# Performance work log

Hardware: AMD Instinct MI355X
Metric: run time of the kernel (lower is better)

The kernel has to match this reference:

```python
import jax, jax.numpy as jnp
import numpy as np

E = 64            # embedding_size
N = 131072        # total nodes (64 states x 2048 objects)
B = 64            # number of states (for readout)
NUM_LAYERS = 2
SMOOTH = 12.0     # MAXIMUM_SMOOTHNESS
RELS = (("r1", 1, 400_000), ("r2", 2, 400_000), ("r3", 3, 150_000))  # (name, arity, n_atoms)


def mish(x):
    return x * jnp.tanh(jax.nn.softplus(x))


def mlp(x, Wi, bi, Wo, bo):
    # MLP: outer(mish(inner(x)))
    return mish(x @ Wi + bi) @ Wo + bo


def setup_inputs() -> dict:
    key = jax.random.key(0)
    ks = iter(jax.random.split(key, 64))

    def lin(i, o):
        s = 1.0 / np.sqrt(i)
        return jax.random.uniform(next(ks), (i, o), jnp.float32, -s, s)

    d = {"node_embeddings": jax.random.normal(next(ks), (N, E), jnp.float32)}
    for r, a, m in RELS:
        d[f"atoms_{r}"] = jax.random.randint(next(ks), (m * a,), 0, N, jnp.int32)
    d["token_sizes"] = jnp.full((B,), N // B, jnp.int32)
    for r, a, _ in RELS:
        sz = a * E
        d[f"Wi_{r}"] = lin(sz, sz); d[f"bi_{r}"] = jnp.zeros((sz,), jnp.float32)
        d[f"Wo_{r}"] = lin(sz, sz); d[f"bo_{r}"] = jnp.zeros((sz,), jnp.float32)
    d["uWi"] = lin(2 * E, 2 * E); d["ubi"] = jnp.zeros((2 * E,), jnp.float32)
    d["uWo"] = lin(2 * E, E);     d["ubo"] = jnp.zeros((E,), jnp.float32)
    for p in ("v", "d"):
        d[f"{p}Wi"] = lin(E, E); d[f"{p}bi"] = jnp.zeros((E,), jnp.float32)
        d[f"{p}Wo"] = lin(E, 1); d[f"{p}bo"] = jnp.zeros((1,), jnp.float32)
    return d


def _layer(h, atoms, rp, uWi, ubi, uWo, ubo):
    # per-relation gather -> residual MLP -> flatten back to per-term messages
    msg_list, idx_list = [], []
    for (r, a, _) in RELS:
        idx = atoms[r]                                  # [m*a] int node ids
        Wi, bi, Wo, bo = rp[r]
        x = h[idx].reshape(-1, a * E)                   # [m, a*E]
        y = x + mlp(x, Wi, bi, Wo, bo)                  # residual relation MLP
        msg_list.append(y.reshape(-1, E))               # [m*a, E]
        idx_list.append(idx)
    msgs = jnp.concatenate(msg_list, 0)                 # [T, E]
    idxs = jnp.concatenate(idx_list, 0)                 # [T]

    # smooth-max aggregation (torch: index_reduce amax under no_grad + stabilized exp-sum-log)
    cnt = jax.ops.segment_sum(jnp.ones((idxs.shape[0], 1), msgs.dtype), idxs, num_segments=N)
    seg_max = jax.ops.segment_max(msgs, idxs, num_segments=N)     # -inf for empty segments
    exps_max = jax.lax.stop_gradient(jnp.where(cnt > 0, seg_max, 0.0))  # include_self=False; empty nodes stay 0
    exps = jnp.exp(SMOOTH * (msgs - exps_max[idxs]))
    exps_sum = 1e-16 + jax.ops.segment_sum(exps, idxs, num_segments=N)
    max_msg = jnp.log(exps_sum) / SMOOTH + exps_max     # [N, E]

    return h + mlp(jnp.concatenate([max_msg, h], 1), uWi, ubi, uWo, ubo)


def _readout(h, token_sizes, Wi, bi, Wo, bo):
    # SumReadout: cumsum-diff segment sums over states, then MLP -> scalar per state
    ci = jnp.cumsum(token_sizes) - 1
    cs = jnp.cumsum(h, axis=0)[ci]                      # [B, E] cumulative sums at segment ends
    agg = jnp.concatenate([cs[:1], cs[1:] - cs[:-1]], 0)
    return mlp(agg, Wi, bi, Wo, bo).reshape(-1)


def _forward(node_embeddings, atoms, token_sizes, params):
    (rp, uWi, ubi, uWo, ubo, vWi, vbi, vWo, vbo, dWi, dbi, dWo, dbo) = params
    h = node_embeddings
    for _ in range(NUM_LAYERS):
        h = _layer(h, atoms, rp, uWi, ubi, uWo, ubo)
    values = _readout(h, token_sizes, vWi, vbi, vWo, vbo)
    deadends = _readout(h, token_sizes, dWi, dbi, dWo, dbo)
    return values, deadends


def reference(node_embeddings, atoms_r1, atoms_r2, atoms_r3, token_sizes,
              Wi_r1, bi_r1, Wo_r1, bo_r1,
              Wi_r2, bi_r2, Wo_r2, bo_r2,
              Wi_r3, bi_r3, Wo_r3, bo_r3,
              uWi, ubi, uWo, ubo,
              vWi, vbi, vWo, vbo,
              dWi, dbi, dWo, dbo):
    atoms = {"r1": atoms_r1, "r2": atoms_r2, "r3": atoms_r3}
    rp = {"r1": (Wi_r1, bi_r1, Wo_r1, bo_r1),
          "r2": (Wi_r2, bi_r2, Wo_r2, bo_r2),
          "r3": (Wi_r3, bi_r3, Wo_r3, bo_r3)}
    params = (rp, uWi, ubi, uWo, ubo, vWi, vbi, vWo, vbo, dWi, dbi, dWo, dbo)
    return _forward(node_embeddings, atoms, token_sizes, params)
```

## Files before the change

kernel.cpp:

```cpp
#include <hip/hip_runtime.h>
#include <math.h>

#define N_NODES 131072
#define NSTATES 64
#define NH ((size_t)N_NODES * 64)

typedef short bf16x8 __attribute__((ext_vector_type(8)));
typedef float f32x4 __attribute__((ext_vector_type(4)));

__device__ __forceinline__ ushort f2bf(float f) {
    unsigned u = __float_as_uint(f);
    return (ushort)((u + 0x7fffu + ((u >> 16) & 1u)) >> 16);
}
__device__ __forceinline__ float bf2f(ushort h) {
    return __uint_as_float(((unsigned)h) << 16);
}
__device__ __forceinline__ float mishf(float x) {
    if (x > 30.f) return x;
    float t = __builtin_amdgcn_exp2f(1.4426950408889634f * x);
    float r = t * t + 2.f * t;
    return x * r * __builtin_amdgcn_rcpf(r + 2.f);
}
__device__ __forceinline__ unsigned enc_f(float f) {
    unsigned u = __float_as_uint(f);
    return (u & 0x80000000u) ? ~u : (u | 0x80000000u);
}
__device__ __forceinline__ float dec_f(unsigned k) {
    unsigned u = (k & 0x80000000u) ? (k & 0x7fffffffu) : ~k;
    return __uint_as_float(u);
}

__device__ __forceinline__ bf16x8 load8f(const float* p) {
    const float4* q = (const float4*)p;
    float4 v0 = q[0], v1 = q[1];
    bf16x8 u;
    u[0] = (short)f2bf(v0.x); u[1] = (short)f2bf(v0.y);
    u[2] = (short)f2bf(v0.z); u[3] = (short)f2bf(v0.w);
    u[4] = (short)f2bf(v1.x); u[5] = (short)f2bf(v1.y);
    u[6] = (short)f2bf(v1.z); u[7] = (short)f2bf(v1.w);
    return u;
}

__global__ __launch_bounds__(256) void h2bf_kernel(
    const float* __restrict__ h, ushort* __restrict__ hb)
{
    size_t i = ((size_t)blockIdx.x * 256 + threadIdx.x) * 8;
    if (i >= NH) return;
    *(bf16x8*)(hb + i) = load8f(h + i);
}

struct WtJob  { const float* src; ushort* dst; int K; int Nc; int start; };
struct WtJobs { WtJob j[8]; int total; };

__global__ __launch_bounds__(256) void wt_conv_all_kernel(WtJobs jobs)
{
    int i = blockIdx.x * 256 + threadIdx.x;
    if (i >= jobs.total) return;
    int jj = 0;
    #pragma unroll
    for (int k = 1; k < 8; k++) if (i >= jobs.j[k].start) jj = k;
    WtJob jb = jobs.j[jj];
    int local = i - jb.start;
    int o = local / jb.K, k = local % jb.K;
    jb.dst[(size_t)o * jb.K + k] = f2bf(jb.src[(size_t)k * jb.Nc + o]);
}

__global__ __launch_bounds__(256) void count_kernel(
    const int* __restrict__ atoms, int T, unsigned* __restrict__ cnt)
{
    int i = blockIdx.x * 256 + threadIdx.x;
    if (i < T) atomicAdd(&cnt[atoms[i]], 1u);
}

__global__ __launch_bounds__(256) void scan1_kernel(
    const unsigned* __restrict__ cnt, unsigned* __restrict__ base,
    unsigned* __restrict__ totals)
{
    __shared__ unsigned sm[256];
    int t = threadIdx.x, blk = blockIdx.x;
    int i0 = blk * 512;
    unsigned a = cnt[i0 + 2 * t], bb = cnt[i0 + 2 * t + 1];
    unsigned p = a + bb;
    sm[t] = p;
    __syncthreads();
    for (int off = 1; off < 256; off <<= 1) {
        unsigned v = (t >= off) ? sm[t - off] : 0u;
        __syncthreads();
        sm[t] += v;
        __syncthreads();
    }
    unsigned incl = sm[t];
    base[i0 + 2 * t]     = incl - p;
    base[i0 + 2 * t + 1] = incl - p + a;
    if (t == 255) totals[blk] = sm[255];
}

__global__ __launch_bounds__(256) void scan2_kernel(
    unsigned* __restrict__ base, unsigned* __restrict__ pos,
    const unsigned* __restrict__ totals)
{
    __shared__ unsigned ps[4];
    int t = threadIdx.x, blk = blockIdx.x;
    int lane = t & 63, wv = t >> 6;
    unsigned v = (t < blk) ? totals[t] : 0u;
    #pragma unroll
    for (int o = 32; o >= 1; o >>= 1) v += (unsigned)__shfl_xor((int)v, o);
    if (lane == 0) ps[wv] = v;
    __syncthreads();
    unsigned off = ps[0] + ps[1] + ps[2] + ps[3];
    int i0 = blk * 512;
    unsigned b0 = base[i0 + 2 * t] + off;
    unsigned b1 = base[i0 + 2 * t + 1] + off;
    base[i0 + 2 * t]     = b0;  pos[i0 + 2 * t]     = b0;
    base[i0 + 2 * t + 1] = b1;  pos[i0 + 2 * t + 1] = b1;
}

template<int ARITY, int MODE>
__global__ __launch_bounds__(256, (ARITY == 3) ? 3 : 4)
void rel_kernel(const ushort* __restrict__ h, const int* __restrict__ atoms,
                const ushort* __restrict__ WiT, const float* __restrict__ bi,
                const ushort* __restrict__ WoT, const float* __restrict__ bo,
                unsigned* __restrict__ pos, ushort* __restrict__ y_sorted,
                unsigned* __restrict__ enc, float* __restrict__ exps, int m)
{
    constexpr int AE  = ARITY * 64;
    constexpr int BM  = 64;
    constexpr int NTW = AE / 64;
    constexpr int KS  = AE / 32;
    constexpr int S   = AE * 2;
    __shared__ __align__(16) ushort xs[BM * AE];
    __shared__ __align__(16) ushort ts[BM * AE];
    __shared__ unsigned slot_sm[BM * ARITY];
    const int tid = threadIdx.x, lane = tid & 63, wv = tid >> 6;
    const int a0 = blockIdx.x * BM;

    for (int task = tid; task < BM * (AE / 8); task += 256) {
        int r  = task / (AE / 8);
        int c8 = task % (AE / 8);
        int atom = a0 + r;
        bf16x8 u = {0, 0, 0, 0, 0, 0, 0, 0};
        if (atom < m) {
            int node = atoms[atom * ARITY + (c8 >> 3)];
            u = *(const bf16x8*)(h + (size_t)node * 64 + (size_t)(c8 & 7) * 8);
        }
        *(bf16x8*)((char*)xs + r * S + ((c8 * 16) ^ ((r & 7) << 4))) = u;
    }
    __syncthreads();

    const int cw0 = wv * NTW * 16;
    const int kg  = (lane >> 4) * 8;
    const int cl  = lane & 15;

    f32x4 acc[4][NTW];
    #pragma unroll
    for (int n = 0; n < NTW; n++) {
        float b = bi[cw0 + n * 16 + cl];
        #pragma unroll
        for (int a = 0; a < 4; a++) acc[a][n] = (f32x4){b, b, b, b};
    }
    #pragma unroll
    for (int ks = 0; ks < KS; ks++) {
        bf16x8 bf[NTW];
        #pragma unroll
        for (int n = 0; n < NTW; n++)
            bf[n] = *(const bf16x8*)(WiT + (size_t)(cw0 + n * 16 + cl) * AE + ks * 32 + kg);
        #pragma unroll
        for (int a = 0; a < 4; a++) {
            int row = a * 16 + cl;
            bf16x8 af = *(const bf16x8*)((char*)xs + row * S + (((ks * 32 + kg) * 2) ^ ((row & 7) << 4)));
            #pragma unroll
            for (int n = 0; n < NTW; n++)
                acc[a][n] = __builtin_amdgcn_mfma_f32_16x16x32_bf16(af, bf[n], acc[a][n], 0, 0, 0);
        }
    }
    #pragma unroll
    for (int a = 0; a < 4; a++)
        #pragma unroll
        for (int n = 0; n < NTW; n++)
            #pragma unroll
            for (int j = 0; j < 4; j++) {
                int row = a * 16 + (lane >> 4) * 4 + j;
                int col = cw0 + n * 16 + cl;
                *(ushort*)((char*)ts + row * S + ((col * 2) ^ ((row & 7) << 4))) = f2bf(mishf(acc[a][n][j]));
            }
    __syncthreads();

    #pragma unroll
    for (int n = 0; n < NTW; n++) {
        float b = bo[cw0 + n * 16 + cl];
        #pragma unroll
        for (int a = 0; a < 4; a++) acc[a][n] = (f32x4){b, b, b, b};
    }
    #pragma unroll
    for (int ks = 0; ks < KS; ks++) {
        bf16x8 bf[NTW];
        #pragma unroll
        for (int n = 0; n < NTW; n++)
            bf[n] = *(const bf16x8*)(WoT + (size_t)(cw0 + n * 16 + cl) * AE + ks * 32 + kg);
        #pragma unroll
        for (int a = 0; a < 4; a++) {
            int row = a * 16 + cl;
            bf16x8 af = *(const bf16x8*)((char*)ts + row * S + (((ks * 32 + kg) * 2) ^ ((row & 7) << 4)));
            #pragma unroll
            for (int n = 0; n < NTW; n++)
                acc[a][n] = __builtin_amdgcn_mfma_f32_16x16x32_bf16(af, bf[n], acc[a][n], 0, 0, 0);
        }
    }
    #pragma unroll
    for (int a = 0; a < 4; a++)
        #pragma unroll
        for (int n = 0; n < NTW; n++)
            #pragma unroll
            for (int j = 0; j < 4; j++) {
                int row = a * 16 + (lane >> 4) * 4 + j;
                int col = cw0 + n * 16 + cl;
                ushort* xp = (ushort*)((char*)xs + row * S + ((col * 2) ^ ((row & 7) << 4)));
                *xp = f2bf(bf2f(*xp) + acc[a][n][j]);
            }
    __syncthreads();

    const int nrows = BM * ARITY;
    if (MODE == 0) {
        if (tid < nrows) {
            int grow = a0 * ARITY + tid;
            unsigned s = 0u;
            if (grow < m * ARITY) s = atomicAdd(&pos[atoms[grow]], 1u);
            slot_sm[tid] = s;
        }
        __syncthreads();
        for (int rr = wv; rr < nrows; rr += 4) {
            int grow = a0 * ARITY + rr;
            if (grow >= m * ARITY) break;
            int r = rr / ARITY, c = (rr % ARITY) * 64 + lane;
            ushort yu = *(ushort*)((char*)xs + r * S + ((c * 2) ^ ((r & 7) << 4)));
            y_sorted[(size_t)slot_sm[rr] * 64 + lane] = yu;
        }
    } else {
        for (int rr = wv; rr < nrows; rr += 4) {
            int grow = a0 * ARITY + rr;
            if (grow >= m * ARITY) break;
            int node = atoms[grow];
            int r = rr / ARITY, c = (rr % ARITY) * 64 + lane;
            ushort yu = *(ushort*)((char*)xs + r * S + ((c * 2) ^ ((r & 7) << 4)));
            if (MODE == 1) {
                atomicMax(&enc[(size_t)node * 64 + lane], enc_f(bf2f(yu)));
            } else {
                size_t cell = (size_t)node * 64 + lane;
                float mx = dec_f(enc[cell]);
                atomicAdd(&exps[cell], __builtin_amdgcn_exp2f(17.312340490667562f * (bf2f(yu) - mx)));
            }
        }
    }
}

#define KSM 17.312340490667562f
__global__ __launch_bounds__(256) void aggregate_kernel(
    const ushort* __restrict__ y_sorted, const unsigned* __restrict__ base,
    const unsigned* __restrict__ cnt, unsigned* __restrict__ pos,
    ushort* __restrict__ mm)
{
    int node = blockIdx.x * 4 + (threadIdx.x >> 6);
    int lane = threadIdx.x & 63;
    unsigned b = base[node], c = cnt[node];
    if (lane == 0) pos[node] = b;
    const ushort* p = y_sorted + (size_t)b * 64 + lane;

    float m = -3.402823466e38f;
    float s = 0.f;
    unsigned j = 0;
    for (; j + 4 <= c; j += 4) {
        float a0 = bf2f(p[(size_t)(j + 0) * 64]);
        float a1 = bf2f(p[(size_t)(j + 1) * 64]);
        float a2 = bf2f(p[(size_t)(j + 2) * 64]);
        float a3 = bf2f(p[(size_t)(j + 3) * 64]);
        float q  = fmaxf(fmaxf(a0, a1), fmaxf(a2, a3));
        float mn = fmaxf(m, q);
        s = s * __builtin_amdgcn_exp2f(KSM * (m - mn))
          + __builtin_amdgcn_exp2f(KSM * (a0 - mn))
          + __builtin_amdgcn_exp2f(KSM * (a1 - mn))
          + __builtin_amdgcn_exp2f(KSM * (a2 - mn))
          + __builtin_amdgcn_exp2f(KSM * (a3 - mn));
        m = mn;
    }
    for (; j < c; j++) {
        float a  = bf2f(p[(size_t)j * 64]);
        float mn = fmaxf(m, a);
        s = s * __builtin_amdgcn_exp2f(KSM * (m - mn))
          + __builtin_amdgcn_exp2f(KSM * (a - mn));
        m = mn;
    }
    float me = c ? m : 0.f;
    float r = __builtin_amdgcn_logf(1e-16f + s) * 0.05776226504666211f + me;
    mm[(size_t)node * 64 + lane] = f2bf(r);
}

__global__ __launch_bounds__(256) void finalize_mm_kernel(
    const unsigned* __restrict__ enc, const float* __restrict__ exps,
    ushort* __restrict__ mm)
{
    size_t i = (size_t)blockIdx.x * 256 + threadIdx.x;
    if (i >= NH) return;
    unsigned key = enc[i];
    float mx = key ? dec_f(key) : 0.f;
    float r = __builtin_amdgcn_logf(1e-16f + exps[i]) * 0.05776226504666211f + mx;
    mm[i] = f2bf(r);
}

__global__ __launch_bounds__(256, 4)
void update_kernel(ushort* __restrict__ hio, const ushort* __restrict__ mm,
                   const ushort* __restrict__ uWiT, const float* __restrict__ ubi,
                   const ushort* __restrict__ uWoT, const float* __restrict__ ubo)
{
    constexpr int AE = 128, BM = 64, S = 256, NTW = 2, KS = 4;
    __shared__ __align__(16) ushort xs[BM * AE];
    __shared__ __align__(16) ushort ts[BM * AE];
    const int tid = threadIdx.x, lane = tid & 63, wv = tid >> 6;
    const int n0 = blockIdx.x * BM;

    for (int task = tid; task < BM * 16; task += 256) {
        int r = task >> 4, c8 = task & 15;
        int node = n0 + r;
        bf16x8 u;
        if (c8 < 8) u = *(const bf16x8*)(mm  + (size_t)node * 64 + c8 * 8);
        else        u = *(const bf16x8*)(hio + (size_t)node * 64 + (size_t)(c8 - 8) * 8);
        *(bf16x8*)((char*)xs + r * S + ((c8 * 16) ^ ((r & 7) << 4))) = u;
    }
    __syncthreads();

    const int cw0 = wv * NTW * 16;
    const int kg  = (lane >> 4) * 8;
    const int cl  = lane & 15;

    f32x4 acc[4][NTW];
    #pragma unroll
    for (int n = 0; n < NTW; n++) {
        float b = ubi[cw0 + n * 16 + cl];
        #pragma unroll
        for (int a = 0; a < 4; a++) acc[a][n] = (f32x4){b, b, b, b};
    }
    #pragma unroll
    for (int ks = 0; ks < KS; ks++) {
        bf16x8 bf[NTW];
        #pragma unroll
        for (int n = 0; n < NTW; n++)
            bf[n] = *(const bf16x8*)(uWiT + (size_t)(cw0 + n * 16 + cl) * AE + ks * 32 + kg);
        #pragma unroll
        for (int a = 0; a < 4; a++) {
            int row = a * 16 + cl;
            bf16x8 af = *(const bf16x8*)((char*)xs + row * S + (((ks * 32 + kg) * 2) ^ ((row & 7) << 4)));
            #pragma unroll
            for (int n = 0; n < NTW; n++)
                acc[a][n] = __builtin_amdgcn_mfma_f32_16x16x32_bf16(af, bf[n], acc[a][n], 0, 0, 0);
        }
    }
    #pragma unroll
    for (int a = 0; a < 4; a++)
        #pragma unroll
        for (int n = 0; n < NTW; n++)
            #pragma unroll
            for (int j = 0; j < 4; j++) {
                int row = a * 16 + (lane >> 4) * 4 + j;
                int col = cw0 + n * 16 + cl;
                *(ushort*)((char*)ts + row * S + ((col * 2) ^ ((row & 7) << 4))) = f2bf(mishf(acc[a][n][j]));
            }
    __syncthreads();

    f32x4 acc2[4];
    {
        float b = ubo[wv * 16 + cl];
        #pragma unroll
        for (int a = 0; a < 4; a++) acc2[a] = (f32x4){b, b, b, b};
    }
    #pragma unroll
    for (int ks = 0; ks < KS; ks++) {
        bf16x8 bf = *(const bf16x8*)(uWoT + (size_t)(wv * 16 + cl) * AE + ks * 32 + kg);
        #pragma unroll
        for (int a = 0; a < 4; a++) {
            int row = a * 16 + cl;
            bf16x8 af = *(const bf16x8*)((char*)ts + row * S + (((ks * 32 + kg) * 2) ^ ((row & 7) << 4)));
            acc2[a] = __builtin_amdgcn_mfma_f32_16x16x32_bf16(af, bf, acc2[a], 0, 0, 0);
        }
    }
    #pragma unroll
    for (int a = 0; a < 4; a++)
        #pragma unroll
        for (int j = 0; j < 4; j++) {
            int row = a * 16 + (lane >> 4) * 4 + j;
            int col = wv * 16 + cl;
            int hc = 64 + col;
            float hold = bf2f(*(ushort*)((char*)xs + row * S + ((hc * 2) ^ ((row & 7) << 4))));
            hio[(size_t)(n0 + row) * 64 + col] = f2bf(hold + acc2[a][j]);
        }
}

__global__ __launch_bounds__(64) void offsets_kernel(
    const int* __restrict__ toksz, int* __restrict__ off)
{
    int lane = threadIdx.x;
    int v = toksz[lane];
    int inc = v;
    #pragma unroll
    for (int o = 1; o < 64; o <<= 1) {
        int t = __shfl_up(inc, o);
        if (lane >= o) inc += t;
    }
    off[lane] = inc - v;
}

#define RCHUNK 32
__global__ __launch_bounds__(256) void readout_partial_kernel(
    const ushort* __restrict__ h, const int* __restrict__ toksz,
    const int* __restrict__ off, float* __restrict__ part)
{
    int s = blockIdx.x >> 5, c = blockIdx.x & (RCHUNK - 1);
    int cntr = toksz[s];
    int rpc = (cntr + RCHUNK - 1) / RCHUNK;
    int r0 = c * rpc;
    int r1 = min(r0 + rpc, cntr);
    int col = threadIdx.x & 63, rg = threadIdx.x >> 6;
    int base = off[s];
    float acc = 0.f;
    for (int r = r0 + rg; r < r1; r += 4)
        acc += bf2f(h[(size_t)(base + r) * 64 + col]);
    __shared__ float red[4][64];
    red[rg][col] = acc;
    __syncthreads();
    if (rg == 0)
        part[(size_t)blockIdx.x * 64 + col] = red[0][col] + red[1][col] + red[2][col] + red[3][col];
}

__global__ __launch_bounds__(256) void readout_reduce_kernel(
    const float* __restrict__ part, float* __restrict__ agg)
{
    int s = blockIdx.x;
    int col = threadIdx.x & 63, rg = threadIdx.x >> 6;
    float acc = 0.f;
    for (int k = rg; k < RCHUNK; k += 4)
        acc += part[(size_t)(s * RCHUNK + k) * 64 + col];
    __shared__ float red[4][64];
    red[rg][col] = acc;
    __syncthreads();
    if (rg == 0)
        agg[s * 64 + col] = red[0][col] + red[1][col] + red[2][col] + red[3][col];
}

__global__ __launch_bounds__(64) void readout_mlp_kernel(
    const float* __restrict__ agg,
    const float* __restrict__ vWi, const float* __restrict__ vbi,
    const float* __restrict__ vWo, const float* __restrict__ vbo,
    const float* __restrict__ dWi, const float* __restrict__ dbi,
    const float* __restrict__ dWo, const float* __restrict__ dbo,
    float* __restrict__ out)
{
    int s = blockIdx.x;
    int lane = threadIdx.x;
    float accv = vbi[lane], accd = dbi[lane];
    for (int k = 0; k < 64; k++) {
        float a = agg[s * 64 + k];
        accv = fmaf(a, vWi[k * 64 + lane], accv);
        accd = fmaf(a, dWi[k * 64 + lane], accd);
    }
    float pv = mishf(accv) * vWo[lane];
    float pd = mishf(accd) * dWo[lane];
    #pragma unroll
    for (int o = 1; o < 64; o <<= 1) {
        pv += __shfl_xor(pv, o);
        pd += __shfl_xor(pd, o);
    }
    if (lane == 0) { out[s] = pv + vbo[0]; out[64 + s] = pd + dbo[0]; }
}

extern "C" void kernel_launch(void* const* d_in, const int* in_sizes, int n_in,
                              void* d_out, int out_size, void* d_ws, size_t ws_size,
                              hipStream_t stream)
{
    const float* h0   = (const float*)d_in[0];
    const int* atoms1 = (const int*)d_in[1];
    const int* atoms2 = (const int*)d_in[2];
    const int* atoms3 = (const int*)d_in[3];
    const int* tsizes = (const int*)d_in[4];
    const float* Wi1 = (const float*)d_in[5],  *bi1 = (const float*)d_in[6];
    const float* Wo1 = (const float*)d_in[7],  *bo1 = (const float*)d_in[8];
    const float* Wi2 = (const float*)d_in[9],  *bi2 = (const float*)d_in[10];
    const float* Wo2 = (const float*)d_in[11], *bo2 = (const float*)d_in[12];
    const float* Wi3 = (const float*)d_in[13], *bi3 = (const float*)d_in[14];
    const float* Wo3 = (const float*)d_in[15], *bo3 = (const float*)d_in[16];
    const float* uWi = (const float*)d_in[17], *ubi = (const float*)d_in[18];
    const float* uWo = (const float*)d_in[19], *ubo = (const float*)d_in[20];
    const float* vWi = (const float*)d_in[21], *vbi = (const float*)d_in[22];
    const float* vWo = (const float*)d_in[23], *vbo = (const float*)d_in[24];
    const float* dWi = (const float*)d_in[25], *dbi = (const float*)d_in[26];
    const float* dWo = (const float*)d_in[27], *dbo = (const float*)d_in[28];
    float* out = (float*)d_out;

    const int rows1 = in_sizes[1];
    const int rows2 = in_sizes[2];
    const int rows3 = in_sizes[3];
    const int m1 = rows1, m2 = rows2 / 2, m3 = rows3 / 3;
    const int T = rows1 + rows2 + rows3;

    char* w = (char*)d_ws;
    auto alloc = [&](size_t bytes) { char* p = w; w += (bytes + 255) & ~(size_t)255; return p; };
    ushort* h1       = (ushort*)alloc(NH * 2);
    ushort* mm       = (ushort*)alloc(NH * 2);
    unsigned* cnt    = (unsigned*)alloc(N_NODES * 4);
    unsigned* base   = (unsigned*)alloc(N_NODES * 4);
    unsigned* pos    = (unsigned*)alloc(N_NODES * 4);
    unsigned* totals = (unsigned*)alloc(256 * 4);
    float* agg       = (float*)alloc(NSTATES * 64 * 4);
    float* part      = (float*)alloc((size_t)NSTATES * RCHUNK * 64 * 4);
    int* roff        = (int*)alloc(NSTATES * 4);
    ushort* WiT1 = (ushort*)alloc(64 * 64 * 2);
    ushort* WoT1 = (ushort*)alloc(64 * 64 * 2);
    ushort* WiT2 = (ushort*)alloc(128 * 128 * 2);
    ushort* WoT2 = (ushort*)alloc(128 * 128 * 2);
    ushort* WiT3 = (ushort*)alloc(192 * 192 * 2);
    ushort* WoT3 = (ushort*)alloc(192 * 192 * 2);
    ushort* uWiT = (ushort*)alloc(128 * 128 * 2);
    ushort* uWoT = (ushort*)alloc(64 * 128 * 2);
    char* tail = w;

    size_t y_bytes  = (size_t)T * 64 * 2;
    const bool csr  = ((size_t)(tail - (char*)d_ws) + ((y_bytes + 255) & ~(size_t)255)) <= ws_size;
    ushort* y_sorted = nullptr;
    unsigned* enc = nullptr;
    float* exps = nullptr;
    if (csr) {
        y_sorted = (ushort*)alloc(y_bytes);
    } else {
        enc  = (unsigned*)alloc(NH * 4);
        exps = (float*)alloc(NH * 4);
    }

    h2bf_kernel<<<(int)(NH / 8 / 256), 256, 0, stream>>>(h0, h1);

    {
        WtJobs jobs;
        int s = 0;
        auto add = [&](int idx, const float* src, ushort* dst, int K, int Nc) {
            jobs.j[idx] = {src, dst, K, Nc, s};
            s += K * Nc;
        };
        add(0, Wi1, WiT1, 64, 64);
        add(1, Wo1, WoT1, 64, 64);
        add(2, Wi2, WiT2, 128, 128);
        add(3, Wo2, WoT2, 128, 128);
        add(4, Wi3, WiT3, 192, 192);
        add(5, Wo3, WoT3, 192, 192);
        add(6, uWi, uWiT, 128, 128);
        add(7, uWo, uWoT, 128, 64);
        jobs.total = s;
        wt_conv_all_kernel<<<(s + 255) / 256, 256, 0, stream>>>(jobs);
    }

    if (csr) {
        hipMemsetAsync(cnt, 0, N_NODES * 4, stream);
        count_kernel<<<(rows1 + 255) / 256, 256, 0, stream>>>(atoms1, rows1, cnt);
        count_kernel<<<(rows2 + 255) / 256, 256, 0, stream>>>(atoms2, rows2, cnt);
        count_kernel<<<(rows3 + 255) / 256, 256, 0, stream>>>(atoms3, rows3, cnt);
        scan1_kernel<<<256, 256, 0, stream>>>(cnt, base, totals);
        scan2_kernel<<<256, 256, 0, stream>>>(base, pos, totals);
    }

    const int g1 = (m1 + 63) / 64, g2 = (m2 + 63) / 64, g3 = (m3 + 63) / 64;

    for (int layer = 0; layer < 2; layer++) {
        if (csr) {
            rel_kernel<1, 0><<<g1, 256, 0, stream>>>(h1, atoms1, WiT1, bi1, WoT1, bo1, pos, y_sorted, nullptr, nullptr, m1);
            rel_kernel<2, 0><<<g2, 256, 0, stream>>>(h1, atoms2, WiT2, bi2, WoT2, bo2, pos, y_sorted, nullptr, nullptr, m2);
            rel_kernel<3, 0><<<g3, 256, 0, stream>>>(h1, atoms3, WiT3, bi3, WoT3, bo3, pos, y_sorted, nullptr, nullptr, m3);
            aggregate_kernel<<<N_NODES / 4, 256, 0, stream>>>(y_sorted, base, cnt, pos, mm);
        } else {
            hipMemsetAsync(enc, 0, NH * 8, stream);
            rel_kernel<1, 1><<<g1, 256, 0, stream>>>(h1, atoms1, WiT1, bi1, WoT1, bo1, nullptr, nullptr, enc, exps, m1);
            rel_kernel<2, 1><<<g2, 256, 0, stream>>>(h1, atoms2, WiT2, bi2, WoT2, bo2, nullptr, nullptr, enc, exps, m2);
            rel_kernel<3, 1><<<g3, 256, 0, stream>>>(h1, atoms3, WiT3, bi3, WoT3, bo3, nullptr, nullptr, enc, exps, m3);
            rel_kernel<1, 2><<<g1, 256, 0, stream>>>(h1, atoms1, WiT1, bi1, WoT1, bo1, nullptr, nullptr, enc, exps, m1);
            rel_kernel<2, 2><<<g2, 256, 0, stream>>>(h1, atoms2, WiT2, bi2, WoT2, bo2, nullptr, nullptr, enc, exps, m2);
            rel_kernel<3, 2><<<g3, 256, 0, stream>>>(h1, atoms3, WiT3, bi3, WoT3, bo3, nullptr, nullptr, enc, exps, m3);
            finalize_mm_kernel<<<(int)((NH + 255) / 256), 256, 0, stream>>>(enc, exps, mm);
        }
        update_kernel<<<N_NODES / 64, 256, 0, stream>>>(h1, mm, uWiT, ubi, uWoT, ubo);
    }

    offsets_kernel<<<1, 64, 0, stream>>>(tsizes, roff);
    readout_partial_kernel<<<NSTATES * RCHUNK, 256, 0, stream>>>(h1, tsizes, roff, part);
    readout_reduce_kernel<<<NSTATES, 256, 0, stream>>>(part, agg);
    readout_mlp_kernel<<<NSTATES, 64, 0, stream>>>(agg, vWi, vbi, vWo, vbo,
                                                   dWi, dbi, dWo, dbo, out);
}
```

Before: 695.3 us.

## Precompute CSR slots once and reuse LDS buffer for hidden activations

Slot assignment for the CSR scatter moves out of the per-layer relation kernels into a one-time rank kernel that stores each term's slot in a buffer. The relation kernels just read this slot, and the aggregate kernel no longer resets pos. For arity 1 and 2, the relation kernel keeps the residual input in registers and overwrites the input LDS buffer with the mish activations, so the second buffer goes away and more blocks fit per CU. The arity-3 kernel keeps two buffers. The cost is more register pressure, an extra slot array, and a new non-deterministic slot order that is fixed once across layers.

```diff
diff --git a/kernel.cpp b/kernel.cpp
--- a/kernel.cpp
+++ b/kernel.cpp
@@ -115,13 +115,21 @@
     base[i0 + 2 * t + 1] = b1;  pos[i0 + 2 * t + 1] = b1;
 }
 
+__global__ __launch_bounds__(256) void rank_kernel(
+    const int* __restrict__ atoms, int T, unsigned* __restrict__ pos,
+    unsigned* __restrict__ slot)
+{
+    int i = blockIdx.x * 256 + threadIdx.x;
+    if (i < T) slot[i] = atomicAdd(&pos[atoms[i]], 1u);
+}
+
 template<int ARITY, int MODE>
-__global__ __launch_bounds__(256, (ARITY == 3) ? 3 : 4)
-void rel_kernel(const ushort* __restrict__ h, const int* __restrict__ atoms,
-                const ushort* __restrict__ WiT, const float* __restrict__ bi,
-                const ushort* __restrict__ WoT, const float* __restrict__ bo,
-                unsigned* __restrict__ pos, ushort* __restrict__ y_sorted,
-                unsigned* __restrict__ enc, float* __restrict__ exps, int m)
+__global__ __launch_bounds__(256, (ARITY == 2) ? 4 : 6)
+void rel_fused_kernel(const ushort* __restrict__ h, const int* __restrict__ atoms,
+                      const ushort* __restrict__ WiT, const float* __restrict__ bi,
+                      const ushort* __restrict__ WoT, const float* __restrict__ bo,
+                      const unsigned* __restrict__ slot, ushort* __restrict__ y_sorted,
+                      unsigned* __restrict__ enc, float* __restrict__ exps, int m)
 {
     constexpr int AE  = ARITY * 64;
     constexpr int BM  = 64;
@@ -129,8 +137,6 @@
     constexpr int KS  = AE / 32;
     constexpr int S   = AE * 2;
     __shared__ __align__(16) ushort xs[BM * AE];
-    __shared__ __align__(16) ushort ts[BM * AE];
-    __shared__ unsigned slot_sm[BM * ARITY];
     const int tid = threadIdx.x, lane = tid & 63, wv = tid >> 6;
     const int a0 = blockIdx.x * BM;
 
@@ -173,6 +179,138 @@
                 acc[a][n] = __builtin_amdgcn_mfma_f32_16x16x32_bf16(af, bf[n], acc[a][n], 0, 0, 0);
         }
     }
+    __syncthreads();
+
+    float xres[4][NTW][4];
+    #pragma unroll
+    for (int a = 0; a < 4; a++)
+        #pragma unroll
+        for (int n = 0; n < NTW; n++)
+            #pragma unroll
+            for (int j = 0; j < 4; j++) {
+                int row = a * 16 + (lane >> 4) * 4 + j;
+                int col = cw0 + n * 16 + cl;
+                ushort* p = (ushort*)((char*)xs + row * S + ((col * 2) ^ ((row & 7) << 4)));
+                xres[a][n][j] = bf2f(*p);
+                *p = f2bf(mishf(acc[a][n][j]));
+            }
+    __syncthreads();
+
+    #pragma unroll
+    for (int n = 0; n < NTW; n++) {
+        float b = bo[cw0 + n * 16 + cl];
+        #pragma unroll
+        for (int a = 0; a < 4; a++) acc[a][n] = (f32x4){b, b, b, b};
+    }
+    #pragma unroll
+    for (int ks = 0; ks < KS; ks++) {
+        bf16x8 bf[NTW];
+        #pragma unroll
+        for (int n = 0; n < NTW; n++)
+            bf[n] = *(const bf16x8*)(WoT + (size_t)(cw0 + n * 16 + cl) * AE + ks * 32 + kg);
+        #pragma unroll
+        for (int a = 0; a < 4; a++) {
+            int row = a * 16 + cl;
+            bf16x8 af = *(const bf16x8*)((char*)xs + row * S + (((ks * 32 + kg) * 2) ^ ((row & 7) << 4)));
+            #pragma unroll
+            for (int n = 0; n < NTW; n++)
+                acc[a][n] = __builtin_amdgcn_mfma_f32_16x16x32_bf16(af, bf[n], acc[a][n], 0, 0, 0);
+        }
+    }
+    __syncthreads();
+
+    #pragma unroll
+    for (int a = 0; a < 4; a++)
+        #pragma unroll
+        for (int n = 0; n < NTW; n++)
+            #pragma unroll
+            for (int j = 0; j < 4; j++) {
+                int row = a * 16 + (lane >> 4) * 4 + j;
+                int col = cw0 + n * 16 + cl;
+                *(ushort*)((char*)xs + row * S + ((col * 2) ^ ((row & 7) << 4))) =
+                    f2bf(xres[a][n][j] + acc[a][n][j]);
+            }
+    __syncthreads();
+
+    const int nrows = BM * ARITY;
+    for (int rr = wv; rr < nrows; rr += 4) {
+        int grow = a0 * ARITY + rr;
+        if (grow >= m * ARITY) break;
+        int r = rr / ARITY, c = (rr % ARITY) * 64 + lane;
+        ushort yu = *(ushort*)((char*)xs + r * S + ((c * 2) ^ ((r & 7) << 4)));
+        if (MODE == 0) {
+            unsigned sl = slot[grow];
+            y_sorted[(size_t)sl * 64 + lane] = yu;
+        } else if (MODE == 1) {
+            int node = atoms[grow];
+            atomicMax(&enc[(size_t)node * 64 + lane], enc_f(bf2f(yu)));
+        } else {
+            int node = atoms[grow];
+            size_t cell = (size_t)node * 64 + lane;
+            float mx = dec_f(enc[cell]);
+            atomicAdd(&exps[cell], __builtin_amdgcn_exp2f(17.312340490667562f * (bf2f(yu) - mx)));
+        }
+    }
+}
+
+template<int MODE>
+__global__ __launch_bounds__(256, 3)
+void rel3_kernel(const ushort* __restrict__ h, const int* __restrict__ atoms,
+                 const ushort* __restrict__ WiT, const float* __restrict__ bi,
+                 const ushort* __restrict__ WoT, const float* __restrict__ bo,
+                 const unsigned* __restrict__ slot, ushort* __restrict__ y_sorted,
+                 unsigned* __restrict__ enc, float* __restrict__ exps, int m)
+{
+    constexpr int ARITY = 3;
+    constexpr int AE  = 192;
+    constexpr int BM  = 64;
+    constexpr int NTW = 3;
+    constexpr int KS  = 6;
+    constexpr int S   = AE * 2;
+    __shared__ __align__(16) ushort xs[BM * AE];
+    __shared__ __align__(16) ushort ts[BM * AE];
+    const int tid = threadIdx.x, lane = tid & 63, wv = tid >> 6;
+    const int a0 = blockIdx.x * BM;
+
+    for (int task = tid; task < BM * (AE / 8); task += 256) {
+        int r  = task / (AE / 8);
+        int c8 = task % (AE / 8);
+        int atom = a0 + r;
+        bf16x8 u = {0, 0, 0, 0, 0, 0, 0, 0};
+        if (atom < m) {
+            int node = atoms[atom * ARITY + (c8 >> 3)];
+            u = *(const bf16x8*)(h + (size_t)node * 64 + (size_t)(c8 & 7) * 8);
+        }
+        *(bf16x8*)((char*)xs + r * S + ((c8 * 16) ^ ((r & 7) << 4))) = u;
+    }
+    __syncthreads();
+
+    const int cw0 = wv * NTW * 16;
+    const int kg  = (lane >> 4) * 8;
+    const int cl  = lane & 15;
+
+    f32x4 acc[4][NTW];
+    #pragma unroll
+    for (int n = 0; n < NTW; n++) {
+        float b = bi[cw0 + n * 16 + cl];
+        #pragma unroll
+        for (int a = 0; a < 4; a++) acc[a][n] = (f32x4){b, b, b, b};
+    }
+    #pragma unroll
+    for (int ks = 0; ks < KS; ks++) {
+        bf16x8 bf[NTW];
+        #pragma unroll
+        for (int n = 0; n < NTW; n++)
+            bf[n] = *(const bf16x8*)(WiT + (size_t)(cw0 + n * 16 + cl) * AE + ks * 32 + kg);
+        #pragma unroll
+        for (int a = 0; a < 4; a++) {
+            int row = a * 16 + cl;
+            bf16x8 af = *(const bf16x8*)((char*)xs + row * S + (((ks * 32 + kg) * 2) ^ ((row & 7) << 4)));
+            #pragma unroll
+            for (int n = 0; n < NTW; n++)
+                acc[a][n] = __builtin_amdgcn_mfma_f32_16x16x32_bf16(af, bf[n], acc[a][n], 0, 0, 0);
+        }
+    }
     #pragma unroll
     for (int a = 0; a < 4; a++)
         #pragma unroll
@@ -220,35 +358,22 @@
     __syncthreads();
 
     const int nrows = BM * ARITY;
-    if (MODE == 0) {
-        if (tid < nrows) {
-            int grow = a0 * ARITY + tid;
-            unsigned s = 0u;
-            if (grow < m * ARITY) s = atomicAdd(&pos[atoms[grow]], 1u);
-            slot_sm[tid] = s;
-        }
-        __syncthreads();
-        for (int rr = wv; rr < nrows; rr += 4) {
-            int grow = a0 * ARITY + rr;
-            if (grow >= m * ARITY) break;
-            int r = rr / ARITY, c = (rr % ARITY) * 64 + lane;
-            ushort yu = *(ushort*)((char*)xs + r * S + ((c * 2) ^ ((r & 7) << 4)));
-            y_sorted[(size_t)slot_sm[rr] * 64 + lane] = yu;
-        }
-    } else {
-        for (int rr = wv; rr < nrows; rr += 4) {
-            int grow = a0 * ARITY + rr;
-            if (grow >= m * ARITY) break;
+    for (int rr = wv; rr < nrows; rr += 4) {
+        int grow = a0 * ARITY + rr;
+        if (grow >= m * ARITY) break;
+        int r = rr / ARITY, c = (rr % ARITY) * 64 + lane;
+        ushort yu = *(ushort*)((char*)xs + r * S + ((c * 2) ^ ((r & 7) << 4)));
+        if (MODE == 0) {
+            unsigned sl = slot[grow];
+            y_sorted[(size_t)sl * 64 + lane] = yu;
+        } else if (MODE == 1) {
             int node = atoms[grow];
-            int r = rr / ARITY, c = (rr % ARITY) * 64 + lane;
-            ushort yu = *(ushort*)((char*)xs + r * S + ((c * 2) ^ ((r & 7) << 4)));
-            if (MODE == 1) {
-                atomicMax(&enc[(size_t)node * 64 + lane], enc_f(bf2f(yu)));
-            } else {
-                size_t cell = (size_t)node * 64 + lane;
-                float mx = dec_f(enc[cell]);
-                atomicAdd(&exps[cell], __builtin_amdgcn_exp2f(17.312340490667562f * (bf2f(yu) - mx)));
-            }
+            atomicMax(&enc[(size_t)node * 64 + lane], enc_f(bf2f(yu)));
+        } else {
+            int node = atoms[grow];
+            size_t cell = (size_t)node * 64 + lane;
+            float mx = dec_f(enc[cell]);
+            atomicAdd(&exps[cell], __builtin_amdgcn_exp2f(17.312340490667562f * (bf2f(yu) - mx)));
         }
     }
 }
@@ -256,13 +381,11 @@
 #define KSM 17.312340490667562f
 __global__ __launch_bounds__(256) void aggregate_kernel(
     const ushort* __restrict__ y_sorted, const unsigned* __restrict__ base,
-    const unsigned* __restrict__ cnt, unsigned* __restrict__ pos,
-    ushort* __restrict__ mm)
+    const unsigned* __restrict__ cnt, ushort* __restrict__ mm)
 {
     int node = blockIdx.x * 4 + (threadIdx.x >> 6);
     int lane = threadIdx.x & 63;
     unsigned b = base[node], c = cnt[node];
-    if (lane == 0) pos[node] = b;
     const ushort* p = y_sorted + (size_t)b * 64 + lane;
 
     float m = -3.402823466e38f;
@@ -507,6 +630,7 @@
     unsigned* base   = (unsigned*)alloc(N_NODES * 4);
     unsigned* pos    = (unsigned*)alloc(N_NODES * 4);
     unsigned* totals = (unsigned*)alloc(256 * 4);
+    unsigned* slot   = (unsigned*)alloc((size_t)T * 4);
     float* agg       = (float*)alloc(NSTATES * 64 * 4);
     float* part      = (float*)alloc((size_t)NSTATES * RCHUNK * 64 * 4);
     int* roff        = (int*)alloc(NSTATES * 4);
@@ -531,6 +655,9 @@
         enc  = (unsigned*)alloc(NH * 4);
         exps = (float*)alloc(NH * 4);
     }
+    unsigned* slot1 = slot;
+    unsigned* slot2 = slot + rows1;
+    unsigned* slot3 = slot + rows1 + rows2;
 
     h2bf_kernel<<<(int)(NH / 8 / 256), 256, 0, stream>>>(h0, h1);
 
@@ -560,24 +687,27 @@
         count_kernel<<<(rows3 + 255) / 256, 256, 0, stream>>>(atoms3, rows3, cnt);
         scan1_kernel<<<256, 256, 0, stream>>>(cnt, base, totals);
         scan2_kernel<<<256, 256, 0, stream>>>(base, pos, totals);
+        rank_kernel<<<(rows1 + 255) / 256, 256, 0, stream>>>(atoms1, rows1, pos, slot1);
+        rank_kernel<<<(rows2 + 255) / 256, 256, 0, stream>>>(atoms2, rows2, pos, slot2);
+        rank_kernel<<<(rows3 + 255) / 256, 256, 0, stream>>>(atoms3, rows3, pos, slot3);
     }
 
     const int g1 = (m1 + 63) / 64, g2 = (m2 + 63) / 64, g3 = (m3 + 63) / 64;
 
     for (int layer = 0; layer < 2; layer++) {
         if (csr) {
-            rel_kernel<1, 0><<<g1, 256, 0, stream>>>(h1, atoms1, WiT1, bi1, WoT1, bo1, pos, y_sorted, nullptr, nullptr, m1);
-            rel_kernel<2, 0><<<g2, 256, 0, stream>>>(h1, atoms2, WiT2, bi2, WoT2, bo2, pos, y_sorted, nullptr, nullptr, m2);
-            rel_kernel<3, 0><<<g3, 256, 0, stream>>>(h1, atoms3, WiT3, bi3, WoT3, bo3, pos, y_sorted, nullptr, nullptr, m3);
-            aggregate_kernel<<<N_NODES / 4, 256, 0, stream>>>(y_sorted, base, cnt, pos, mm);
+            rel_fused_kernel<1, 0><<<g1, 256, 0, stream>>>(h1, atoms1, WiT1, bi1, WoT1, bo1, slot1, y_sorted, nullptr, nullptr, m1);
+            rel_fused_kernel<2, 0><<<g2, 256, 0, stream>>>(h1, atoms2, WiT2, bi2, WoT2, bo2, slot2, y_sorted, nullptr, nullptr, m2);
+            rel3_kernel<0><<<g3, 256, 0, stream>>>(h1, atoms3, WiT3, bi3, WoT3, bo3, slot3, y_sorted, nullptr, nullptr, m3);
+            aggregate_kernel<<<N_NODES / 4, 256, 0, stream>>>(y_sorted, base, cnt, mm);
         } else {
             hipMemsetAsync(enc, 0, NH * 8, stream);
-            rel_kernel<1, 1><<<g1, 256, 0, stream>>>(h1, atoms1, WiT1, bi1, WoT1, bo1, nullptr, nullptr, enc, exps, m1);
-            rel_kernel<2, 1><<<g2, 256, 0, stream>>>(h1, atoms2, WiT2, bi2, WoT2, bo2, nullptr, nullptr, enc, exps, m2);
-            rel_kernel<3, 1><<<g3, 256, 0, stream>>>(h1, atoms3, WiT3, bi3, WoT3, bo3, nullptr, nullptr, enc, exps, m3);
-            rel_kernel<1, 2><<<g1, 256, 0, stream>>>(h1, atoms1, WiT1, bi1, WoT1, bo1, nullptr, nullptr, enc, exps, m1);
-            rel_kernel<2, 2><<<g2, 256, 0, stream>>>(h1, atoms2, WiT2, bi2, WoT2, bo2, nullptr, nullptr, enc, exps, m2);
-            rel_kernel<3, 2><<<g3, 256, 0, stream>>>(h1, atoms3, WiT3, bi3, WoT3, bo3, nullptr, nullptr, enc, exps, m3);
+            rel_fused_kernel<1, 1><<<g1, 256, 0, stream>>>(h1, atoms1, WiT1, bi1, WoT1, bo1, nullptr, nullptr, enc, exps, m1);
+            rel_fused_kernel<2, 1><<<g2, 256, 0, stream>>>(h1, atoms2, WiT2, bi2, WoT2, bo2, nullptr, nullptr, enc, exps, m2);
+            rel3_kernel<1><<<g3, 256, 0, stream>>>(h1, atoms3, WiT3, bi3, WoT3, bo3, nullptr, nullptr, enc, exps, m3);
+            rel_fused_kernel<1, 2><<<g1, 256, 0, stream>>>(h1, atoms1, WiT1, bi1, WoT1, bo1, nullptr, nullptr, enc, exps, m1);
+            rel_fused_kernel<2, 2><<<g2, 256, 0, stream>>>(h1, atoms2, WiT2, bi2, WoT2, bo2, nullptr, nullptr, enc, exps, m2);
+            rel3_kernel<2><<<g3, 256, 0, stream>>>(h1, atoms3, WiT3, bi3, WoT3, bo3, nullptr, nullptr, enc, exps, m3);
             finalize_mm_kernel<<<(int)((NH + 255) / 256), 256, 0, stream>>>(enc, exps, mm);
         }
         update_kernel<<<N_NODES / 64, 256, 0, stream>>>(h1, mm, uWiT, ubi, uWoT, ubo);
```

New measurement: 837.9 us. 1.21x slower.
